# Performance work log

Measured on AMD Instinct MI355X. Metric: run time of the kernel, lower is better.

## Reference

```python
import jax, jax.numpy as jnp
import numpy as np

N_USERS = 100000
N_LOCAS = 50000
N = N_USERS + N_LOCAS
D = 128   # embedding_dynamic_size
K = 128   # kg entity dim
S = 128   # static dim
NK = 50000  # kg rows
E = 2048  # number of events
LN_EPS = 1e-5
NORM_EPS = 1e-12


def setup_inputs() -> dict:
    key = jax.random.key(0)
    ks = jax.random.split(key, 24)
    f = jnp.float32
    rin = D + K + 1
    s_rnn = 1.0 / np.sqrt(D)
    s_pred = 1.0 / np.sqrt(2 * S + 2 * D + K)
    inp = {
        'embedding': jax.random.normal(ks[0], (N, D), f),
        'static': jax.random.normal(ks[1], (N, S), f),
        'kg': jax.random.normal(ks[2], (NK, K), f),
        'W_ih_u': jax.random.normal(ks[3], (D, rin), f) * s_rnn,
        'b_ih_u': jax.random.normal(ks[4], (D,), f) * s_rnn,
        'W_hh_u': jax.random.normal(ks[5], (D, D), f) * s_rnn,
        'b_hh_u': jax.random.normal(ks[6], (D,), f) * s_rnn,
        'W_ih_l': jax.random.normal(ks[7], (D, rin), f) * s_rnn,
        'b_ih_l': jax.random.normal(ks[8], (D,), f) * s_rnn,
        'W_hh_l': jax.random.normal(ks[9], (D, D), f) * s_rnn,
        'b_hh_l': jax.random.normal(ks[10], (D,), f) * s_rnn,
        'w_proj': jax.random.normal(ks[11], (D,), f),   # NormalLinear(1, D) weight, std=1/sqrt(1)=1
        'b_proj': jax.random.normal(ks[12], (D,), f),
        'ln_g': jnp.ones((D + K,), f),
        'ln_b': jnp.zeros((D + K,), f),
        'W_pred': jax.random.normal(ks[13], (S + D, 2 * S + 2 * D + K), f) * s_pred,
        'b_pred': jnp.zeros((S + D,), f),
        'delta_u': jax.random.uniform(ks[14], (E,), f),
        'delta_l': jax.random.uniform(ks[15], (E,), f),
        'idx_user': jax.random.randint(ks[16], (E,), 0, N_USERS, jnp.int32),
        'idx_loca': jax.random.randint(ks[17], (E,), 0, N_LOCAS, jnp.int32),
        'idx_prev': jax.random.randint(ks[18], (E,), 0, N_LOCAS, jnp.int32),
        'idx_know': jax.random.randint(ks[19], (E,), 0, NK, jnp.int32),
        'num_users': N_USERS,
    }
    return inp


def reference(embedding, static, kg, W_ih_u, b_ih_u, W_hh_u, b_hh_u,
              W_ih_l, b_ih_l, W_hh_l, b_hh_l, w_proj, b_proj, ln_g, ln_b,
              W_pred, b_pred, delta_u, delta_l,
              idx_user, idx_loca, idx_prev, idx_know, num_users):
    sg = jax.lax.stop_gradient

    def l2n(x):  # F.normalize along the feature dim (row vector)
        return x / jnp.maximum(jnp.linalg.norm(x), NORM_EPS)

    # event index preprocessing (matches idx_loca + num_users etc.)
    xs = (idx_user, idx_loca + num_users, idx_prev + num_users, idx_know,
          delta_u, delta_l)

    def step(carry, ev):
        emb, loss = carry
        iu, il, ip, ik, du, dl = ev
        u = emb[iu]        # [D]
        l = emb[il]        # [D]
        p = emb[ip]        # [D]
        kgr = kg[ik]       # [K]
        # projection: u * (1 + Linear(1->D)(delta_u))
        proj = u * (1.0 + w_proj * du + b_proj)
        # layer_norm over concat([emb_prev, kg_row]) of size D+K
        x = jnp.concatenate([p, kgr])
        mu = x.mean()
        var = jnp.mean((x - mu) ** 2)
        ln = (x - mu) / jnp.sqrt(var + LN_EPS) * ln_g + ln_b
        meta = jnp.concatenate([proj, ln, static[ip], static[iu]])  # [2S+2D+K]
        pred = W_pred @ meta + b_pred                               # [S+D]
        tgt = jnp.concatenate([l, static[il]])
        loss_pred = jnp.mean((pred - sg(tgt)) ** 2)
        # RNNCell updates (tanh), then L2-normalize
        x_u = jnp.concatenate([l, kgr, du[None]])
        new_u = l2n(jnp.tanh(W_ih_u @ x_u + b_ih_u + W_hh_u @ u + b_hh_u))
        x_l = jnp.concatenate([u, kgr, dl[None]])
        new_l = l2n(jnp.tanh(W_ih_l @ x_l + b_ih_l + W_hh_l @ l + b_hh_l))
        loss = loss + loss_pred \
                    + jnp.mean((new_u - sg(u)) ** 2) \
                    + jnp.mean((new_l - sg(l)) ** 2)
        emb = emb.at[iu].set(new_u).at[il].set(new_l)
        return (emb, loss), None

    (emb, loss), _ = jax.lax.scan(
        step, (embedding, jnp.asarray(0.0, embedding.dtype)), xs)
    return emb, loss
```

## Files before the change

### kernel.cpp

```cpp
#include <hip/hip_runtime.h>

#define DEVINL static __device__ __forceinline__

typedef float f32x4 __attribute__((ext_vector_type(4)));

constexpr int NUSER = 100000;
constexpr int D     = 128;
constexpr int METAN = 640;
constexpr int NT    = 256;
constexpr int CH    = 4;
constexpr int KP4   = 160;
constexpr int KR4   = 96;
constexpr int NCPY  = 2048;
constexpr int NINIT = 512;
constexpr int CIW   = 20;

struct Params {
  const float *emb_in, *stat, *kg;
  const float *Wihu, *bihu, *Whhu, *bhhu;
  const float *Wihl, *bihl, *Whhl, *bhhl;
  const float *wproj, *bproj, *lng, *lnb, *Wpred, *bpred;
  const float *deltau, *deltal;
  const int *idxu, *idxl, *idxp, *idxk;
  float *emb;
  float *loss_slot;
  float *WpredT;
  float *WrnnT;
  float *brnn;
  float *wcol;
  float *loss_ev;
  int *cinfo;
  int *cnt_u, *cnt_w, *cnt_t;
  int *flag_u, *flag_l;
  int E, N, NLOC, NWORK;
};

DEVINL float loadx(const float* p) {
  return __hip_atomic_load(p, __ATOMIC_RELAXED, __HIP_MEMORY_SCOPE_AGENT);
}
DEVINL void storex(float* p, float v) {
  __hip_atomic_store(p, v, __ATOMIC_RELAXED, __HIP_MEMORY_SCOPE_AGENT);
}
DEVINL int loadcnt(const int* p) {
  return __hip_atomic_load(p, __ATOMIC_RELAXED, __HIP_MEMORY_SCOPE_AGENT);
}
DEVINL void sigadd(int* pp) {
  __hip_atomic_fetch_add(pp, 1, __ATOMIC_RELAXED, __HIP_MEMORY_SCOPE_AGENT);
}
DEVINL float dot4(float4 a, float4 b) { return a.x*b.x + a.y*b.y + a.z*b.z + a.w*b.w; }

DEVINL float4 block_sum4(float4 v, float4* s4) {
  #pragma unroll
  for (int o = 32; o; o >>= 1) {
    v.x += __shfl_xor(v.x, o, 64); v.y += __shfl_xor(v.y, o, 64);
    v.z += __shfl_xor(v.z, o, 64); v.w += __shfl_xor(v.w, o, 64);
  }
  if ((threadIdx.x & 63) == 0) s4[threadIdx.x >> 6] = v;
  __syncthreads();
  float4 r;
  r.x = s4[0].x + s4[1].x + s4[2].x + s4[3].x;
  r.y = s4[0].y + s4[1].y + s4[2].y + s4[3].y;
  r.z = s4[0].z + s4[1].z + s4[2].z + s4[3].z;
  r.w = s4[0].w + s4[1].w + s4[2].w + s4[3].w;
  __syncthreads();
  return r;
}

DEVINL void half_sum4(float4 v, float4* s4, float4* lo, float4* hi) {
  #pragma unroll
  for (int o = 32; o; o >>= 1) {
    v.x += __shfl_xor(v.x, o, 64); v.y += __shfl_xor(v.y, o, 64);
    v.z += __shfl_xor(v.z, o, 64); v.w += __shfl_xor(v.w, o, 64);
  }
  if ((threadIdx.x & 63) == 0) s4[threadIdx.x >> 6] = v;
  __syncthreads();
  lo->x = s4[0].x + s4[1].x; lo->y = s4[0].y + s4[1].y;
  lo->z = s4[0].z + s4[1].z; lo->w = s4[0].w + s4[1].w;
  hi->x = s4[2].x + s4[3].x; hi->y = s4[2].y + s4[3].y;
  hi->z = s4[2].z + s4[3].z; hi->w = s4[2].w + s4[3].w;
  __syncthreads();
}

__global__ __launch_bounds__(NT) void k_prep(Params p) {
  const int tid = threadIdx.x, w = tid >> 6, lane = tid & 63;
  const int bid = blockIdx.x;

  if (bid >= p.NWORK) {
    int gid = (bid - p.NWORK) * NT + tid;
    int stride = NINIT * NT;
    for (int e = gid; e < p.E; e += stride) {
      p.flag_u[p.idxu[e]] = 1;
      p.flag_l[p.idxl[e]] = 1;
    }
    for (int idx = gid; idx < 256 * KP4; idx += stride) {
      int j = idx / KP4, k4 = idx - j * KP4;
      float4 v = *(const float4*)(p.Wpred + (size_t)j * METAN + k4 * 4);
      ((float4*)p.WpredT)[k4 * 256 + j] = v;
    }
    for (int idx = gid; idx < 256 * KR4; idx += stride) {
      int j = idx / KR4, k4 = idx - j * KR4;
      int i = j & 127;
      const float* Wih = (j < 128) ? p.Wihu : p.Wihl;
      const float* Whh = (j < 128) ? p.Whhu : p.Whhl;
      float4 v; float* vp = (float*)&v;
      #pragma unroll
      for (int e = 0; e < 4; ++e) {
        int k = k4 * 4 + e;
        vp[e] = (k < 256) ? Wih[(size_t)i * 257 + k] : Whh[(size_t)i * 128 + (k - 256)];
      }
      ((float4*)p.WrnnT)[k4 * 256 + j] = v;
    }
    for (int j = gid; j < 256; j += stride) {
      int i = j & 127;
      p.brnn[j] = (j < 128) ? p.bihu[i] + p.bhhu[i] : p.bihl[i] + p.bhhl[i];
      p.wcol[j] = (j < 128) ? p.Wihu[(size_t)i * 257 + 256] : p.Wihl[(size_t)i * 257 + 256];
    }
    return;
  }

  __shared__ unsigned long long s_redu[4][CH];
  const int c = bid, base = c * CH;
  const int nev = min(CH, p.E - base);
  if (nev <= 0) return;

  int iu_[CH], il_[CH], ip_[CH];
  #pragma unroll
  for (int e = 0; e < CH; ++e) {
    int t = base + e; bool v = e < nev;
    iu_[e] = v ? p.idxu[t] : -1;
    il_[e] = v ? p.idxl[t] : -1;
    ip_[e] = v ? p.idxp[t] : -1;
  }
  unsigned long long pk[CH] = {0ull,0ull,0ull,0ull};
  for (int s = tid; s < base; s += NT) {
    int ius = p.idxu[s], ils = p.idxl[s], ips = p.idxp[s];
    #pragma unroll
    for (int e = 0; e < CH; ++e) {
      unsigned long long a  = (ius == iu_[e]);
      unsigned long long wl = (ils == il_[e]);
      unsigned long long b  = (unsigned long long)((ils == il_[e]) + (ips == il_[e]));
      unsigned long long cc = (ils == ip_[e]);
      pk[e] += a | (wl << 16) | (b << 32) | (cc << 48);
    }
  }
  #pragma unroll
  for (int o = 32; o; o >>= 1) {
    #pragma unroll
    for (int e = 0; e < CH; ++e) pk[e] += __shfl_xor(pk[e], o, 64);
  }
  if (lane == 0) {
    #pragma unroll
    for (int e = 0; e < CH; ++e) s_redu[w][e] = pk[e];
  }
  __syncthreads();
  #pragma unroll
  for (int e = 0; e < CH; ++e)
    pk[e] = s_redu[0][e] + s_redu[1][e] + s_redu[2][e] + s_redu[3][e];

  if (tid == 0) {
    int* ci = p.cinfo + (size_t)c * CIW;
    bool internal = false;
    #pragma unroll
    for (int t2 = 1; t2 < CH; ++t2) if (t2 < nev) {
      #pragma unroll
      for (int s2 = 0; s2 < t2; ++s2)
        internal |= (iu_[s2] == iu_[t2]) | (il_[s2] == il_[t2]) |
                    (il_[s2] == ip_[t2]) | (ip_[s2] == il_[t2]);
    }
    bool clean = !internal;
    #pragma unroll
    for (int e = 0; e < CH; ++e) {
      int a  = (int)(pk[e] & 0xffff),        wl = (int)((pk[e] >> 16) & 0xffff);
      int b  = (int)((pk[e] >> 32) & 0xffff), cc = (int)((pk[e] >> 48) & 0xffff);
      #pragma unroll
      for (int s2 = 0; s2 < CH; ++s2) if (s2 < e) {
        a  += (iu_[s2] == iu_[e]);
        wl += (il_[s2] == il_[e]);
        b  += (il_[s2] == il_[e]) + (ip_[s2] == il_[e]);
        cc += (il_[s2] == ip_[e]);
      }
      ci[e] = a; ci[4 + e] = wl; ci[8 + e] = b; ci[12 + e] = cc;
      if (e < nev) clean = clean && (a == 0) && (b == 0) && (cc == 0);
    }
    ci[16] = internal ? 1 : 0;
    ci[17] = clean ? 1 : 0;
  }
}

__global__ __launch_bounds__(NT, 2) void k_main(Params p) {
  const int tid = threadIdx.x, w = tid >> 6, lane = tid & 63;
  const int bid = blockIdx.x;

  if (bid >= p.NWORK) {
    size_t gid = (size_t)(bid - p.NWORK) * NT + tid;
    size_t gs  = (size_t)NCPY * NT;
    size_t n4  = (size_t)p.N * 32;
    const f32x4* src = (const f32x4*)p.emb_in;
    f32x4* dst = (f32x4*)p.emb;
    size_t g = gid;
    for (; g + 3 * gs < n4; g += 4 * gs) {
      size_t g0 = g, g1 = g + gs, g2 = g + 2 * gs, g3 = g + 3 * gs;
      int r0 = (int)(g0 >> 5), r1 = (int)(g1 >> 5), r2 = (int)(g2 >> 5), r3 = (int)(g3 >> 5);
      int f0 = (r0 < NUSER) ? p.flag_u[r0] : p.flag_l[r0 - NUSER];
      int f1 = (r1 < NUSER) ? p.flag_u[r1] : p.flag_l[r1 - NUSER];
      int f2 = (r2 < NUSER) ? p.flag_u[r2] : p.flag_l[r2 - NUSER];
      int f3 = (r3 < NUSER) ? p.flag_u[r3] : p.flag_l[r3 - NUSER];
      f32x4 v0 = src[g0], v1 = src[g1], v2 = src[g2], v3 = src[g3];
      if (!f0) dst[g0] = v0;
      if (!f1) dst[g1] = v1;
      if (!f2) dst[g2] = v2;
      if (!f3) dst[g3] = v3;
    }
    for (; g < n4; g += gs) {
      int r = (int)(g >> 5);
      int f = (r < NUSER) ? p.flag_u[r] : p.flag_l[r - NUSER];
      f32x4 v = src[g];
      if (!f) dst[g] = v;
    }
    return;
  }

  __shared__ __align__(16) float s_meta[CH][METAN];
  __shared__ __align__(16) float s_u[CH][D], s_l[CH][D], s_p[CH][D], s_kg[CH][D], s_sil[CH][D];
  __shared__ float4 s_r4[4];
  __shared__ int s_ev[8][CH];
  __shared__ float s_dd[2][CH];

  const int c = bid, base = c * CH;
  const int nev = min(CH, p.E - base);
  if (nev <= 0) return;
  const int* ci = p.cinfo + (size_t)c * CIW;
  const int internal = ci[16];
  const int clean    = ci[17];

  if (tid == 0) {
    #pragma unroll
    for (int e = 0; e < CH; ++e) {
      int t = base + e; bool v = e < nev;
      s_ev[0][e] = v ? p.idxu[t] : 0;
      s_ev[1][e] = v ? p.idxl[t] : 0;
      s_ev[2][e] = v ? p.idxp[t] : 0;
      s_ev[3][e] = ci[e];
      s_ev[4][e] = ci[4 + e];
      s_ev[5][e] = ci[8 + e];
      s_ev[6][e] = ci[12 + e];
      s_ev[7][e] = v ? p.idxk[t] : 0;
      s_dd[0][e] = v ? p.deltau[t] : 0.f;
      s_dd[1][e] = v ? p.deltal[t] : 0.f;
    }
  }
  __syncthreads();

  if (w < nev) {
    int e = w;
    int iu = s_ev[0][e], ilr = s_ev[1][e] + NUSER, ipr = s_ev[2][e] + NUSER;
    int A = s_ev[3][e], WL = s_ev[4][e], Ck = s_ev[6][e], ik = s_ev[7][e];
    int h2 = lane >> 5, li = (lane & 31) * 4;
    if (h2 == 0) {
      *(float4*)&s_kg[e][li]         = *(const float4*)(p.kg   + (size_t)ik  * D + li);
      *(float4*)&s_meta[e][512 + li] = *(const float4*)(p.stat + (size_t)iu  * D + li);
    } else {
      *(float4*)&s_meta[e][384 + li] = *(const float4*)(p.stat + (size_t)ipr * D + li);
      *(float4*)&s_sil[e][li]        = *(const float4*)(p.stat + (size_t)ilr * D + li);
    }
    int i0 = lane * 2;
    if (!A)  *(float2*)&s_u[e][i0] = *(const float2*)(p.emb_in + (size_t)iu  * D + i0);
    if (!WL) *(float2*)&s_l[e][i0] = *(const float2*)(p.emb_in + (size_t)ilr * D + i0);
    if (!Ck) *(float2*)&s_p[e][i0] = *(const float2*)(p.emb_in + (size_t)ipr * D + i0);
  }

  auto SPIN = [&](int b0, int b1) {
    if (w == 0) {
      int e = b0 + lane;
      bool act = lane < (b1 - b0);
      int iu = 0, il = 0, ip = 0, A = 0, Bc = 0, Cc = 0;
      if (act) {
        iu = s_ev[0][e]; il = s_ev[1][e]; ip = s_ev[2][e];
        A = s_ev[3][e]; Bc = s_ev[5][e]; Cc = s_ev[6][e];
      }
      int guard = 0;
      while (true) {
        int x = loadcnt(&p.cnt_u[iu]);
        int y = loadcnt(&p.cnt_t[il]);
        int z = loadcnt(&p.cnt_w[ip]);
        bool ok = (!act) | ((x >= A) & (y >= Bc) & (z >= Cc));
        if (__all(ok)) break;
        if (++guard > (1 << 22)) break;
        __builtin_amdgcn_s_sleep(1);
      }
    }
    __syncthreads();
  };

  auto POSTLOAD = [&](int b0, int b1) {
    int e = w;
    if (e >= b0 && e < b1) {
      int iu = s_ev[0][e], ilr = s_ev[1][e] + NUSER, ipr = s_ev[2][e] + NUSER;
      int A = s_ev[3][e], WL = s_ev[4][e], Ck = s_ev[6][e];
      int i0 = lane * 2;
      if (A) {
        s_u[e][i0]   = loadx(p.emb + (size_t)iu * D + i0);
        s_u[e][i0+1] = loadx(p.emb + (size_t)iu * D + i0 + 1);
      }
      if (WL) {
        s_l[e][i0]   = loadx(p.emb + (size_t)ilr * D + i0);
        s_l[e][i0+1] = loadx(p.emb + (size_t)ilr * D + i0 + 1);
      }
      if (Ck) {
        s_p[e][i0]   = loadx(p.emb + (size_t)ipr * D + i0);
        s_p[e][i0+1] = loadx(p.emb + (size_t)ipr * D + i0 + 1);
      }
    }
  };

  float nvkeep[CH] = {0.f, 0.f, 0.f, 0.f};
  const bool uc = (tid < 128);

  auto RNNPROC = [&](int b0, int b1) {
    __syncthreads();
    const float4* xo0 = (const float4*)(uc ? s_l[0] : s_u[0]);
    const float4* xo1 = (const float4*)(uc ? s_l[1] : s_u[1]);
    const float4* xo2 = (const float4*)(uc ? s_l[2] : s_u[2]);
    const float4* xo3 = (const float4*)(uc ? s_l[3] : s_u[3]);
    const float4* xk0 = (const float4*)s_kg[0];
    const float4* xk1 = (const float4*)s_kg[1];
    const float4* xk2 = (const float4*)s_kg[2];
    const float4* xk3 = (const float4*)s_kg[3];
    const float4* xs0 = (const float4*)(uc ? s_u[0] : s_l[0]);
    const float4* xs1 = (const float4*)(uc ? s_u[1] : s_l[1]);
    const float4* xs2 = (const float4*)(uc ? s_u[2] : s_l[2]);
    const float4* xs3 = (const float4*)(uc ? s_u[3] : s_l[3]);
    float ra0 = 0.f, ra1 = 0.f, ra2 = 0.f, ra3 = 0.f;
    const float4* wr = (const float4*)p.WrnnT + tid;
    #pragma unroll 8
    for (int k4 = 0; k4 < 32; ++k4) {
      float4 wv = wr[k4 * 256];
      ra0 += dot4(wv, xo0[k4]); ra1 += dot4(wv, xo1[k4]);
      ra2 += dot4(wv, xo2[k4]); ra3 += dot4(wv, xo3[k4]);
    }
    #pragma unroll 8
    for (int k4 = 32; k4 < 64; ++k4) {
      float4 wv = wr[k4 * 256];
      ra0 += dot4(wv, xk0[k4-32]); ra1 += dot4(wv, xk1[k4-32]);
      ra2 += dot4(wv, xk2[k4-32]); ra3 += dot4(wv, xk3[k4-32]);
    }
    #pragma unroll 8
    for (int k4 = 64; k4 < 96; ++k4) {
      float4 wv = wr[k4 * 256];
      ra0 += dot4(wv, xs0[k4-64]); ra1 += dot4(wv, xs1[k4-64]);
      ra2 += dot4(wv, xs2[k4-64]); ra3 += dot4(wv, xs3[k4-64]);
    }
    float brn = p.brnn[tid], wcv = p.wcol[tid];
    float d0 = uc ? s_dd[0][0] : s_dd[1][0];
    float d1 = uc ? s_dd[0][1] : s_dd[1][1];
    float d2 = uc ? s_dd[0][2] : s_dd[1][2];
    float d3 = uc ? s_dd[0][3] : s_dd[1][3];
    float h0 = tanhf(ra0 + brn + wcv * d0), h1 = tanhf(ra1 + brn + wcv * d1);
    float h2v = tanhf(ra2 + brn + wcv * d2), h3 = tanhf(ra3 + brn + wcv * d3);

    float4 SU, SL;
    half_sum4(make_float4(h0*h0, h1*h1, h2v*h2v, h3*h3), s_r4, &SU, &SL);
    float s0 = uc ? SU.x : SL.x, s1 = uc ? SU.y : SL.y;
    float s2 = uc ? SU.z : SL.z, s3 = uc ? SU.w : SL.w;
    float n0 = h0 / fmaxf(sqrtf(s0), 1e-12f), n1 = h1 / fmaxf(sqrtf(s1), 1e-12f);
    float n2 = h2v / fmaxf(sqrtf(s2), 1e-12f), n3 = h3 / fmaxf(sqrtf(s3), 1e-12f);

    if (b0 <= 0 && 0 < b1) nvkeep[0] = n0;
    if (b0 <= 1 && 1 < b1) nvkeep[1] = n1;
    if (b0 <= 2 && 2 < b1) nvkeep[2] = n2;
    if (b0 <= 3 && 3 < b1) nvkeep[3] = n3;

    float nv[CH] = {n0, n1, n2, n3};
    #pragma unroll
    for (int e = 0; e < CH; ++e) if (e >= b0 && e < b1) {
      if (tid < 128) storex(p.emb + (size_t)s_ev[0][e] * D + tid, nv[e]);
      else           storex(p.emb + ((size_t)s_ev[1][e] + NUSER) * D + (tid - 128), nv[e]);
    }
    __syncthreads();

    if (tid >= b0 && tid < b1) {
      __builtin_amdgcn_fence(__ATOMIC_RELEASE, "agent");
      sigadd(&p.cnt_u[s_ev[0][tid]]);
      sigadd(&p.cnt_t[s_ev[1][tid]]);
      sigadd(&p.cnt_w[s_ev[1][tid]]);
      sigadd(&p.cnt_t[s_ev[2][tid]]);
    }
  };

  if (clean) {
    RNNPROC(0, nev);
  } else if (!internal) {
    SPIN(0, nev);
    POSTLOAD(0, nev);
    RNNPROC(0, nev);
  } else {
    #pragma unroll
    for (int e = 0; e < CH; ++e) {
      if (e < nev) {
        SPIN(e, e + 1);
        POSTLOAD(e, e + 1);
        RNNPROC(e, e + 1);
      }
    }
  }

  if (w < nev) {
    int e = w;
    float du = s_dd[0][e];
    float4 xv = (lane < 32) ? *(const float4*)&s_p[e][lane * 4]
                            : *(const float4*)&s_kg[e][(lane - 32) * 4];
    float sm = xv.x + xv.y + xv.z + xv.w;
    #pragma unroll
    for (int o = 32; o; o >>= 1) sm += __shfl_xor(sm, o, 64);
    float mu = sm * (1.f / 256.f);
    float4 d = make_float4(xv.x - mu, xv.y - mu, xv.z - mu, xv.w - mu);
    float vs = d.x*d.x + d.y*d.y + d.z*d.z + d.w*d.w;
    #pragma unroll
    for (int o = 32; o; o >>= 1) vs += __shfl_xor(vs, o, 64);
    float rstd = rsqrtf(vs * (1.f / 256.f) + 1e-5f);
    int idx2 = lane * 4;
    float4 g  = *(const float4*)&p.lng[idx2];
    float4 bb = *(const float4*)&p.lnb[idx2];
    *(float4*)&s_meta[e][128 + idx2] = make_float4(
      d.x*rstd*g.x + bb.x, d.y*rstd*g.y + bb.y,
      d.z*rstd*g.z + bb.z, d.w*rstd*g.w + bb.w);
    int i0 = lane * 2;
    #pragma unroll
    for (int j = 0; j < 2; ++j) {
      int i = i0 + j;
      s_meta[e][i] = s_u[e][i] * (1.f + p.wproj[i] * du + p.bproj[i]);
    }
  }
  __syncthreads();

  const float4* m40 = (const float4*)&s_meta[0][0];
  const float4* m41 = (const float4*)&s_meta[1][0];
  const float4* m42 = (const float4*)&s_meta[2][0];
  const float4* m43 = (const float4*)&s_meta[3][0];
  float pa0 = 0.f, pa1 = 0.f, pa2 = 0.f, pa3 = 0.f;
  const float4* wp = (const float4*)p.WpredT + tid;
  #pragma unroll 8
  for (int k4 = 0; k4 < KP4; ++k4) {
    float4 wv = wp[k4 * 256];
    pa0 += dot4(wv, m40[k4]); pa1 += dot4(wv, m41[k4]);
    pa2 += dot4(wv, m42[k4]); pa3 += dot4(wv, m43[k4]);
  }
  float bp = p.bpred[tid];
  float4 ep2;
  {
    float tg0 = uc ? s_l[0][tid] : s_sil[0][tid - 128];
    float tg1 = uc ? s_l[1][tid] : s_sil[1][tid - 128];
    float tg2 = uc ? s_l[2][tid] : s_sil[2][tid - 128];
    float tg3 = uc ? s_l[3][tid] : s_sil[3][tid - 128];
    float e0 = pa0 + bp - tg0, e1 = pa1 + bp - tg1;
    float e2 = pa2 + bp - tg2, e3 = pa3 + bp - tg3;
    ep2 = make_float4(e0*e0, e1*e1, e2*e2, e3*e3);
  }
  float4 LP = block_sum4(ep2, s_r4);

  float o0 = uc ? s_u[0][tid] : s_l[0][tid - 128];
  float o1 = uc ? s_u[1][tid] : s_l[1][tid - 128];
  float o2 = uc ? s_u[2][tid] : s_l[2][tid - 128];
  float o3 = uc ? s_u[3][tid] : s_l[3][tid - 128];
  float q0 = nvkeep[0] - o0, q1 = nvkeep[1] - o1;
  float q2 = nvkeep[2] - o2, q3 = nvkeep[3] - o3;
  float4 LE = block_sum4(make_float4(q0*q0, q1*q1, q2*q2, q3*q3), s_r4);

  if (tid < nev) {
    float lp = (tid == 0) ? LP.x : (tid == 1) ? LP.y : (tid == 2) ? LP.z : LP.w;
    float le = (tid == 0) ? LE.x : (tid == 1) ? LE.y : (tid == 2) ? LE.z : LE.w;
    p.loss_ev[base + tid] = lp * (1.f / 256.f) + le * (1.f / 128.f);
  }
}

__global__ void k_fin(Params p) {
  __shared__ float4 s_r4[4];
  float v = 0.f;
  for (int i = threadIdx.x; i < p.E; i += NT) v += p.loss_ev[i];
  float4 r = block_sum4(make_float4(v, 0.f, 0.f, 0.f), s_r4);
  if (threadIdx.x == 0) p.loss_slot[0] = r.x;
}

extern "C" void kernel_launch(void* const* d_in, const int* in_sizes, int n_in,
                              void* d_out, int out_size, void* d_ws, size_t ws_size,
                              hipStream_t stream) {
  Params p;
  p.emb_in = (const float*)d_in[0];
  p.stat   = (const float*)d_in[1];
  p.kg     = (const float*)d_in[2];
  p.Wihu = (const float*)d_in[3];   p.bihu = (const float*)d_in[4];
  p.Whhu = (const float*)d_in[5];   p.bhhu = (const float*)d_in[6];
  p.Wihl = (const float*)d_in[7];   p.bihl = (const float*)d_in[8];
  p.Whhl = (const float*)d_in[9];   p.bhhl = (const float*)d_in[10];
  p.wproj = (const float*)d_in[11]; p.bproj = (const float*)d_in[12];
  p.lng  = (const float*)d_in[13];  p.lnb  = (const float*)d_in[14];
  p.Wpred = (const float*)d_in[15]; p.bpred = (const float*)d_in[16];
  p.deltau = (const float*)d_in[17];
  p.deltal = (const float*)d_in[18];
  p.idxu = (const int*)d_in[19];
  p.idxl = (const int*)d_in[20];
  p.idxp = (const int*)d_in[21];
  p.idxk = (const int*)d_in[22];

  p.E    = in_sizes[17];
  p.N    = in_sizes[0] / D;
  p.NLOC = p.N - NUSER;
  p.NWORK = (p.E + CH - 1) / CH;

  p.emb       = (float*)d_out;
  p.loss_slot = (float*)d_out + (size_t)p.N * D;

  char* ws = (char*)d_ws;
  size_t off = 0;
  auto take = [&](size_t bytes) {
    void* r = ws + off;
    off += (bytes + 255) & ~(size_t)255;
    return r;
  };
  p.WpredT  = (float*)take((size_t)KP4 * 256 * 16);
  p.WrnnT   = (float*)take((size_t)KR4 * 256 * 16);
  p.brnn    = (float*)take(256 * 4);
  p.wcol    = (float*)take(256 * 4);
  p.loss_ev = (float*)take((size_t)p.E * 4);
  p.cinfo   = (int*)take((size_t)p.NWORK * CIW * 4);
  size_t z0 = off;
  p.cnt_u   = (int*)take((size_t)NUSER * 4);
  p.cnt_w   = (int*)take((size_t)p.NLOC * 4);
  p.cnt_t   = (int*)take((size_t)p.NLOC * 4);
  p.flag_u  = (int*)take((size_t)NUSER * 4);
  p.flag_l  = (int*)take((size_t)p.NLOC * 4);
  size_t zbytes = off - z0;

  hipMemsetAsync(ws + z0, 0, zbytes, stream);
  hipLaunchKernelGGL(k_prep, dim3(p.NWORK + NINIT), dim3(NT), 0, stream, p);
  hipLaunchKernelGGL(k_main, dim3(p.NWORK + NCPY),  dim3(NT), 0, stream, p);
  hipLaunchKernelGGL(k_fin,  dim3(1),               dim3(NT), 0, stream, p);
}
```

Before: 151.5 us.

## Split prediction-loss work into separate blocks off the recurrent critical path

Worker blocks now do only the RNN update and dependency signalling. They stash their inputs and new states to a workspace buffer and set a per-chunk done flag. A second set of blocks waits on that flag, reloads the stash, and computes the layer norm, the prediction matvec and the losses, so that work no longer delays the serial chain of dependent events. The copy grid is halved to make room for the extra blocks. This adds stash traffic and spin-waiting blocks that occupy CUs, and the design relies on worker blocks being scheduled before the loss blocks.

```diff
diff --git a/kernel.cpp b/kernel.cpp
--- a/kernel.cpp
+++ b/kernel.cpp
@@ -11,8 +11,9 @@
 constexpr int CH    = 4;
 constexpr int KP4   = 160;
 constexpr int KR4   = 96;
-constexpr int NCPY  = 2048;
+constexpr int NCPY  = 1024;
 constexpr int NINIT = 512;
+constexpr int STW   = 640;
 constexpr int CIW   = 20;
 
 struct Params {
@@ -29,9 +30,11 @@
   float *brnn;
   float *wcol;
   float *loss_ev;
+  float *stash;
   int *cinfo;
   int *cnt_u, *cnt_w, *cnt_t;
   int *flag_u, *flag_l;
+  int *done;
   int E, N, NLOC, NWORK;
 };
 
@@ -43,6 +46,9 @@
 }
 DEVINL int loadcnt(const int* p) {
   return __hip_atomic_load(p, __ATOMIC_RELAXED, __HIP_MEMORY_SCOPE_AGENT);
+}
+DEVINL void storei(int* p, int v) {
+  __hip_atomic_store(p, v, __ATOMIC_RELAXED, __HIP_MEMORY_SCOPE_AGENT);
 }
 DEVINL void sigadd(int* pp) {
   __hip_atomic_fetch_add(pp, 1, __ATOMIC_RELAXED, __HIP_MEMORY_SCOPE_AGENT);
@@ -188,10 +194,16 @@
 }
 
 __global__ __launch_bounds__(NT, 2) void k_main(Params p) {
+  __shared__ __align__(16) float s_meta[CH][METAN];
+  __shared__ __align__(16) float s_u[CH][D], s_l[CH][D], s_p[CH][D], s_kg[CH][D], s_sil[CH][D];
+  __shared__ float4 s_r4[4];
+  __shared__ int s_ev[8][CH];
+  __shared__ float s_dd[2][CH];
+
   const int tid = threadIdx.x, w = tid >> 6, lane = tid & 63;
   const int bid = blockIdx.x;
 
-  if (bid >= p.NWORK) {
+  if (bid >= p.NWORK && bid < p.NWORK + NCPY) {
     size_t gid = (size_t)(bid - p.NWORK) * NT + tid;
     size_t gs  = (size_t)NCPY * NT;
     size_t n4  = (size_t)p.N * 32;
@@ -220,256 +232,300 @@
     return;
   }
 
-  __shared__ __align__(16) float s_meta[CH][METAN];
-  __shared__ __align__(16) float s_u[CH][D], s_l[CH][D], s_p[CH][D], s_kg[CH][D], s_sil[CH][D];
-  __shared__ float4 s_r4[4];
-  __shared__ int s_ev[8][CH];
-  __shared__ float s_dd[2][CH];
-
-  const int c = bid, base = c * CH;
+  const bool is_worker = (bid < p.NWORK);
+  const int c = is_worker ? bid : bid - p.NWORK - NCPY;
+  const int base = c * CH;
   const int nev = min(CH, p.E - base);
   if (nev <= 0) return;
-  const int* ci = p.cinfo + (size_t)c * CIW;
-  const int internal = ci[16];
-  const int clean    = ci[17];
-
-  if (tid == 0) {
-    #pragma unroll
-    for (int e = 0; e < CH; ++e) {
-      int t = base + e; bool v = e < nev;
-      s_ev[0][e] = v ? p.idxu[t] : 0;
-      s_ev[1][e] = v ? p.idxl[t] : 0;
-      s_ev[2][e] = v ? p.idxp[t] : 0;
-      s_ev[3][e] = ci[e];
-      s_ev[4][e] = ci[4 + e];
-      s_ev[5][e] = ci[8 + e];
-      s_ev[6][e] = ci[12 + e];
-      s_ev[7][e] = v ? p.idxk[t] : 0;
-      s_dd[0][e] = v ? p.deltau[t] : 0.f;
-      s_dd[1][e] = v ? p.deltal[t] : 0.f;
-    }
-  }
-  __syncthreads();
-
-  if (w < nev) {
-    int e = w;
-    int iu = s_ev[0][e], ilr = s_ev[1][e] + NUSER, ipr = s_ev[2][e] + NUSER;
-    int A = s_ev[3][e], WL = s_ev[4][e], Ck = s_ev[6][e], ik = s_ev[7][e];
-    int h2 = lane >> 5, li = (lane & 31) * 4;
-    if (h2 == 0) {
-      *(float4*)&s_kg[e][li]         = *(const float4*)(p.kg   + (size_t)ik  * D + li);
-      *(float4*)&s_meta[e][512 + li] = *(const float4*)(p.stat + (size_t)iu  * D + li);
+
+  if (is_worker) {
+    const int* ci = p.cinfo + (size_t)c * CIW;
+    const int internal = ci[16];
+    const int clean    = ci[17];
+
+    if (tid == 0) {
+      #pragma unroll
+      for (int e = 0; e < CH; ++e) {
+        int t = base + e; bool v = e < nev;
+        s_ev[0][e] = v ? p.idxu[t] : 0;
+        s_ev[1][e] = v ? p.idxl[t] : 0;
+        s_ev[2][e] = v ? p.idxp[t] : 0;
+        s_ev[3][e] = ci[e];
+        s_ev[4][e] = ci[4 + e];
+        s_ev[5][e] = ci[8 + e];
+        s_ev[6][e] = ci[12 + e];
+        s_ev[7][e] = v ? p.idxk[t] : 0;
+        s_dd[0][e] = v ? p.deltau[t] : 0.f;
+        s_dd[1][e] = v ? p.deltal[t] : 0.f;
+      }
+    }
+    __syncthreads();
+
+    if (w < nev) {
+      int e = w;
+      int iu = s_ev[0][e], ilr = s_ev[1][e] + NUSER, ipr = s_ev[2][e] + NUSER;
+      int A = s_ev[3][e], WL = s_ev[4][e], Ck = s_ev[6][e], ik = s_ev[7][e];
+      if (lane < 32) {
+        int li = lane * 4;
+        *(float4*)&s_kg[e][li] = *(const float4*)(p.kg + (size_t)ik * D + li);
+      }
+      int i0 = lane * 2;
+      if (!A)  *(float2*)&s_u[e][i0] = *(const float2*)(p.emb_in + (size_t)iu  * D + i0);
+      if (!WL) *(float2*)&s_l[e][i0] = *(const float2*)(p.emb_in + (size_t)ilr * D + i0);
+      if (!Ck) *(float2*)&s_p[e][i0] = *(const float2*)(p.emb_in + (size_t)ipr * D + i0);
+    }
+
+    auto SPIN = [&](int b0, int b1) {
+      if (w == 0) {
+        int e = b0 + lane;
+        bool act = lane < (b1 - b0);
+        int iu = 0, il = 0, ip = 0, A = 0, Bc = 0, Cc = 0;
+        if (act) {
+          iu = s_ev[0][e]; il = s_ev[1][e]; ip = s_ev[2][e];
+          A = s_ev[3][e]; Bc = s_ev[5][e]; Cc = s_ev[6][e];
+        }
+        int guard = 0;
+        while (true) {
+          int x = loadcnt(&p.cnt_u[iu]);
+          int y = loadcnt(&p.cnt_t[il]);
+          int z = loadcnt(&p.cnt_w[ip]);
+          bool ok = (!act) | ((x >= A) & (y >= Bc) & (z >= Cc));
+          if (__all(ok)) break;
+          if (++guard > (1 << 22)) break;
+          __builtin_amdgcn_s_sleep(1);
+        }
+      }
+      __syncthreads();
+    };
+
+    auto POSTLOAD = [&](int b0, int b1) {
+      int e = w;
+      if (e >= b0 && e < b1) {
+        int iu = s_ev[0][e], ilr = s_ev[1][e] + NUSER, ipr = s_ev[2][e] + NUSER;
+        int A = s_ev[3][e], WL = s_ev[4][e], Ck = s_ev[6][e];
+        int i0 = lane * 2;
+        if (A) {
+          s_u[e][i0]   = loadx(p.emb + (size_t)iu * D + i0);
+          s_u[e][i0+1] = loadx(p.emb + (size_t)iu * D + i0 + 1);
+        }
+        if (WL) {
+          s_l[e][i0]   = loadx(p.emb + (size_t)ilr * D + i0);
+          s_l[e][i0+1] = loadx(p.emb + (size_t)ilr * D + i0 + 1);
+        }
+        if (Ck) {
+          s_p[e][i0]   = loadx(p.emb + (size_t)ipr * D + i0);
+          s_p[e][i0+1] = loadx(p.emb + (size_t)ipr * D + i0 + 1);
+        }
+      }
+    };
+
+    const bool uc = (tid < 128);
+    auto RNNPROC = [&](int b0, int b1) {
+      __syncthreads();
+      const float4* xo0 = (const float4*)(uc ? s_l[0] : s_u[0]);
+      const float4* xo1 = (const float4*)(uc ? s_l[1] : s_u[1]);
+      const float4* xo2 = (const float4*)(uc ? s_l[2] : s_u[2]);
+      const float4* xo3 = (const float4*)(uc ? s_l[3] : s_u[3]);
+      const float4* xk0 = (const float4*)s_kg[0];
+      const float4* xk1 = (const float4*)s_kg[1];
+      const float4* xk2 = (const float4*)s_kg[2];
+      const float4* xk3 = (const float4*)s_kg[3];
+      const float4* xs0 = (const float4*)(uc ? s_u[0] : s_l[0]);
+      const float4* xs1 = (const float4*)(uc ? s_u[1] : s_l[1]);
+      const float4* xs2 = (const float4*)(uc ? s_u[2] : s_l[2]);
+      const float4* xs3 = (const float4*)(uc ? s_u[3] : s_l[3]);
+      float ra0 = 0.f, ra1 = 0.f, ra2 = 0.f, ra3 = 0.f;
+      const float4* wr = (const float4*)p.WrnnT + tid;
+      #pragma unroll 8
+      for (int k4 = 0; k4 < 32; ++k4) {
+        float4 wv = wr[k4 * 256];
+        ra0 += dot4(wv, xo0[k4]); ra1 += dot4(wv, xo1[k4]);
+        ra2 += dot4(wv, xo2[k4]); ra3 += dot4(wv, xo3[k4]);
+      }
+      #pragma unroll 8
+      for (int k4 = 32; k4 < 64; ++k4) {
+        float4 wv = wr[k4 * 256];
+        ra0 += dot4(wv, xk0[k4-32]); ra1 += dot4(wv, xk1[k4-32]);
+        ra2 += dot4(wv, xk2[k4-32]); ra3 += dot4(wv, xk3[k4-32]);
+      }
+      #pragma unroll 8
+      for (int k4 = 64; k4 < 96; ++k4) {
+        float4 wv = wr[k4 * 256];
+        ra0 += dot4(wv, xs0[k4-64]); ra1 += dot4(wv, xs1[k4-64]);
+        ra2 += dot4(wv, xs2[k4-64]); ra3 += dot4(wv, xs3[k4-64]);
+      }
+      float brn = p.brnn[tid], wcv = p.wcol[tid];
+      float d0 = uc ? s_dd[0][0] : s_dd[1][0];
+      float d1 = uc ? s_dd[0][1] : s_dd[1][1];
+      float d2 = uc ? s_dd[0][2] : s_dd[1][2];
+      float d3 = uc ? s_dd[0][3] : s_dd[1][3];
+      float h0 = tanhf(ra0 + brn + wcv * d0), h1 = tanhf(ra1 + brn + wcv * d1);
+      float h2v = tanhf(ra2 + brn + wcv * d2), h3 = tanhf(ra3 + brn + wcv * d3);
+
+      float4 SU, SL;
+      half_sum4(make_float4(h0*h0, h1*h1, h2v*h2v, h3*h3), s_r4, &SU, &SL);
+      float s0 = uc ? SU.x : SL.x, s1 = uc ? SU.y : SL.y;
+      float s2 = uc ? SU.z : SL.z, s3 = uc ? SU.w : SL.w;
+      float n0 = h0 / fmaxf(sqrtf(s0), 1e-12f), n1 = h1 / fmaxf(sqrtf(s1), 1e-12f);
+      float n2 = h2v / fmaxf(sqrtf(s2), 1e-12f), n3 = h3 / fmaxf(sqrtf(s3), 1e-12f);
+
+      float nv[CH] = {n0, n1, n2, n3};
+      #pragma unroll
+      for (int e = 0; e < CH; ++e) if (e >= b0 && e < b1) {
+        if (tid < 128) storex(p.emb + (size_t)s_ev[0][e] * D + tid, nv[e]);
+        else           storex(p.emb + ((size_t)s_ev[1][e] + NUSER) * D + (tid - 128), nv[e]);
+      }
+      __syncthreads();
+
+      if (tid >= b0 && tid < b1) {
+        __builtin_amdgcn_fence(__ATOMIC_RELEASE, "agent");
+        sigadd(&p.cnt_u[s_ev[0][tid]]);
+        sigadd(&p.cnt_t[s_ev[1][tid]]);
+        sigadd(&p.cnt_w[s_ev[1][tid]]);
+        sigadd(&p.cnt_t[s_ev[2][tid]]);
+      }
+
+      #pragma unroll
+      for (int e = 0; e < CH; ++e) if (e >= b0 && e < b1) {
+        float* st = p.stash + (size_t)(base + e) * STW;
+        if (tid < 128) {
+          storex(st + tid,       s_u[e][tid]);
+          storex(st + 256 + tid, s_p[e][tid]);
+          storex(st + 384 + tid, nv[e]);
+        } else {
+          int i = tid - 128;
+          storex(st + 128 + i, s_l[e][i]);
+          storex(st + 512 + i, nv[e]);
+        }
+      }
+    };
+
+    if (clean) {
+      RNNPROC(0, nev);
+    } else if (!internal) {
+      SPIN(0, nev);
+      POSTLOAD(0, nev);
+      RNNPROC(0, nev);
     } else {
-      *(float4*)&s_meta[e][384 + li] = *(const float4*)(p.stat + (size_t)ipr * D + li);
-      *(float4*)&s_sil[e][li]        = *(const float4*)(p.stat + (size_t)ilr * D + li);
-    }
-    int i0 = lane * 2;
-    if (!A)  *(float2*)&s_u[e][i0] = *(const float2*)(p.emb_in + (size_t)iu  * D + i0);
-    if (!WL) *(float2*)&s_l[e][i0] = *(const float2*)(p.emb_in + (size_t)ilr * D + i0);
-    if (!Ck) *(float2*)&s_p[e][i0] = *(const float2*)(p.emb_in + (size_t)ipr * D + i0);
-  }
-
-  auto SPIN = [&](int b0, int b1) {
-    if (w == 0) {
-      int e = b0 + lane;
-      bool act = lane < (b1 - b0);
-      int iu = 0, il = 0, ip = 0, A = 0, Bc = 0, Cc = 0;
-      if (act) {
-        iu = s_ev[0][e]; il = s_ev[1][e]; ip = s_ev[2][e];
-        A = s_ev[3][e]; Bc = s_ev[5][e]; Cc = s_ev[6][e];
-      }
-      int guard = 0;
-      while (true) {
-        int x = loadcnt(&p.cnt_u[iu]);
-        int y = loadcnt(&p.cnt_t[il]);
-        int z = loadcnt(&p.cnt_w[ip]);
-        bool ok = (!act) | ((x >= A) & (y >= Bc) & (z >= Cc));
-        if (__all(ok)) break;
-        if (++guard > (1 << 22)) break;
-        __builtin_amdgcn_s_sleep(1);
-      }
-    }
-    __syncthreads();
-  };
-
-  auto POSTLOAD = [&](int b0, int b1) {
-    int e = w;
-    if (e >= b0 && e < b1) {
-      int iu = s_ev[0][e], ilr = s_ev[1][e] + NUSER, ipr = s_ev[2][e] + NUSER;
-      int A = s_ev[3][e], WL = s_ev[4][e], Ck = s_ev[6][e];
-      int i0 = lane * 2;
-      if (A) {
-        s_u[e][i0]   = loadx(p.emb + (size_t)iu * D + i0);
-        s_u[e][i0+1] = loadx(p.emb + (size_t)iu * D + i0 + 1);
-      }
-      if (WL) {
-        s_l[e][i0]   = loadx(p.emb + (size_t)ilr * D + i0);
-        s_l[e][i0+1] = loadx(p.emb + (size_t)ilr * D + i0 + 1);
-      }
-      if (Ck) {
-        s_p[e][i0]   = loadx(p.emb + (size_t)ipr * D + i0);
-        s_p[e][i0+1] = loadx(p.emb + (size_t)ipr * D + i0 + 1);
-      }
-    }
-  };
-
-  float nvkeep[CH] = {0.f, 0.f, 0.f, 0.f};
-  const bool uc = (tid < 128);
-
-  auto RNNPROC = [&](int b0, int b1) {
-    __syncthreads();
-    const float4* xo0 = (const float4*)(uc ? s_l[0] : s_u[0]);
-    const float4* xo1 = (const float4*)(uc ? s_l[1] : s_u[1]);
-    const float4* xo2 = (const float4*)(uc ? s_l[2] : s_u[2]);
-    const float4* xo3 = (const float4*)(uc ? s_l[3] : s_u[3]);
-    const float4* xk0 = (const float4*)s_kg[0];
-    const float4* xk1 = (const float4*)s_kg[1];
-    const float4* xk2 = (const float4*)s_kg[2];
-    const float4* xk3 = (const float4*)s_kg[3];
-    const float4* xs0 = (const float4*)(uc ? s_u[0] : s_l[0]);
-    const float4* xs1 = (const float4*)(uc ? s_u[1] : s_l[1]);
-    const float4* xs2 = (const float4*)(uc ? s_u[2] : s_l[2]);
-    const float4* xs3 = (const float4*)(uc ? s_u[3] : s_l[3]);
-    float ra0 = 0.f, ra1 = 0.f, ra2 = 0.f, ra3 = 0.f;
-    const float4* wr = (const float4*)p.WrnnT + tid;
-    #pragma unroll 8
-    for (int k4 = 0; k4 < 32; ++k4) {
-      float4 wv = wr[k4 * 256];
-      ra0 += dot4(wv, xo0[k4]); ra1 += dot4(wv, xo1[k4]);
-      ra2 += dot4(wv, xo2[k4]); ra3 += dot4(wv, xo3[k4]);
-    }
-    #pragma unroll 8
-    for (int k4 = 32; k4 < 64; ++k4) {
-      float4 wv = wr[k4 * 256];
-      ra0 += dot4(wv, xk0[k4-32]); ra1 += dot4(wv, xk1[k4-32]);
-      ra2 += dot4(wv, xk2[k4-32]); ra3 += dot4(wv, xk3[k4-32]);
-    }
-    #pragma unroll 8
-    for (int k4 = 64; k4 < 96; ++k4) {
-      float4 wv = wr[k4 * 256];
-      ra0 += dot4(wv, xs0[k4-64]); ra1 += dot4(wv, xs1[k4-64]);
-      ra2 += dot4(wv, xs2[k4-64]); ra3 += dot4(wv, xs3[k4-64]);
-    }
-    float brn = p.brnn[tid], wcv = p.wcol[tid];
-    float d0 = uc ? s_dd[0][0] : s_dd[1][0];
-    float d1 = uc ? s_dd[0][1] : s_dd[1][1];
-    float d2 = uc ? s_dd[0][2] : s_dd[1][2];
-    float d3 = uc ? s_dd[0][3] : s_dd[1][3];
-    float h0 = tanhf(ra0 + brn + wcv * d0), h1 = tanhf(ra1 + brn + wcv * d1);
-    float h2v = tanhf(ra2 + brn + wcv * d2), h3 = tanhf(ra3 + brn + wcv * d3);
-
-    float4 SU, SL;
-    half_sum4(make_float4(h0*h0, h1*h1, h2v*h2v, h3*h3), s_r4, &SU, &SL);
-    float s0 = uc ? SU.x : SL.x, s1 = uc ? SU.y : SL.y;
-    float s2 = uc ? SU.z : SL.z, s3 = uc ? SU.w : SL.w;
-    float n0 = h0 / fmaxf(sqrtf(s0), 1e-12f), n1 = h1 / fmaxf(sqrtf(s1), 1e-12f);
-    float n2 = h2v / fmaxf(sqrtf(s2), 1e-12f), n3 = h3 / fmaxf(sqrtf(s3), 1e-12f);
-
-    if (b0 <= 0 && 0 < b1) nvkeep[0] = n0;
-    if (b0 <= 1 && 1 < b1) nvkeep[1] = n1;
-    if (b0 <= 2 && 2 < b1) nvkeep[2] = n2;
-    if (b0 <= 3 && 3 < b1) nvkeep[3] = n3;
-
-    float nv[CH] = {n0, n1, n2, n3};
-    #pragma unroll
-    for (int e = 0; e < CH; ++e) if (e >= b0 && e < b1) {
-      if (tid < 128) storex(p.emb + (size_t)s_ev[0][e] * D + tid, nv[e]);
-      else           storex(p.emb + ((size_t)s_ev[1][e] + NUSER) * D + (tid - 128), nv[e]);
-    }
-    __syncthreads();
-
-    if (tid >= b0 && tid < b1) {
-      __builtin_amdgcn_fence(__ATOMIC_RELEASE, "agent");
-      sigadd(&p.cnt_u[s_ev[0][tid]]);
-      sigadd(&p.cnt_t[s_ev[1][tid]]);
-      sigadd(&p.cnt_w[s_ev[1][tid]]);
-      sigadd(&p.cnt_t[s_ev[2][tid]]);
-    }
-  };
-
-  if (clean) {
-    RNNPROC(0, nev);
-  } else if (!internal) {
-    SPIN(0, nev);
-    POSTLOAD(0, nev);
-    RNNPROC(0, nev);
-  } else {
-    #pragma unroll
-    for (int e = 0; e < CH; ++e) {
-      if (e < nev) {
+      #pragma unroll
+      for (int e = 0; e < CH; ++e) if (e < nev) {
         SPIN(e, e + 1);
         POSTLOAD(e, e + 1);
         RNNPROC(e, e + 1);
       }
     }
-  }
-
-  if (w < nev) {
-    int e = w;
-    float du = s_dd[0][e];
-    float4 xv = (lane < 32) ? *(const float4*)&s_p[e][lane * 4]
-                            : *(const float4*)&s_kg[e][(lane - 32) * 4];
-    float sm = xv.x + xv.y + xv.z + xv.w;
-    #pragma unroll
-    for (int o = 32; o; o >>= 1) sm += __shfl_xor(sm, o, 64);
-    float mu = sm * (1.f / 256.f);
-    float4 d = make_float4(xv.x - mu, xv.y - mu, xv.z - mu, xv.w - mu);
-    float vs = d.x*d.x + d.y*d.y + d.z*d.z + d.w*d.w;
-    #pragma unroll
-    for (int o = 32; o; o >>= 1) vs += __shfl_xor(vs, o, 64);
-    float rstd = rsqrtf(vs * (1.f / 256.f) + 1e-5f);
-    int idx2 = lane * 4;
-    float4 g  = *(const float4*)&p.lng[idx2];
-    float4 bb = *(const float4*)&p.lnb[idx2];
-    *(float4*)&s_meta[e][128 + idx2] = make_float4(
-      d.x*rstd*g.x + bb.x, d.y*rstd*g.y + bb.y,
-      d.z*rstd*g.z + bb.z, d.w*rstd*g.w + bb.w);
-    int i0 = lane * 2;
-    #pragma unroll
-    for (int j = 0; j < 2; ++j) {
-      int i = i0 + j;
-      s_meta[e][i] = s_u[e][i] * (1.f + p.wproj[i] * du + p.bproj[i]);
-    }
-  }
-  __syncthreads();
-
-  const float4* m40 = (const float4*)&s_meta[0][0];
-  const float4* m41 = (const float4*)&s_meta[1][0];
-  const float4* m42 = (const float4*)&s_meta[2][0];
-  const float4* m43 = (const float4*)&s_meta[3][0];
-  float pa0 = 0.f, pa1 = 0.f, pa2 = 0.f, pa3 = 0.f;
-  const float4* wp = (const float4*)p.WpredT + tid;
-  #pragma unroll 8
-  for (int k4 = 0; k4 < KP4; ++k4) {
-    float4 wv = wp[k4 * 256];
-    pa0 += dot4(wv, m40[k4]); pa1 += dot4(wv, m41[k4]);
-    pa2 += dot4(wv, m42[k4]); pa3 += dot4(wv, m43[k4]);
-  }
-  float bp = p.bpred[tid];
-  float4 ep2;
+    __syncthreads();
+    if (tid == 0) storei(&p.done[c], 1);
+    return;
+  }
+
   {
-    float tg0 = uc ? s_l[0][tid] : s_sil[0][tid - 128];
-    float tg1 = uc ? s_l[1][tid] : s_sil[1][tid - 128];
-    float tg2 = uc ? s_l[2][tid] : s_sil[2][tid - 128];
-    float tg3 = uc ? s_l[3][tid] : s_sil[3][tid - 128];
-    float e0 = pa0 + bp - tg0, e1 = pa1 + bp - tg1;
-    float e2 = pa2 + bp - tg2, e3 = pa3 + bp - tg3;
-    ep2 = make_float4(e0*e0, e1*e1, e2*e2, e3*e3);
-  }
-  float4 LP = block_sum4(ep2, s_r4);
-
-  float o0 = uc ? s_u[0][tid] : s_l[0][tid - 128];
-  float o1 = uc ? s_u[1][tid] : s_l[1][tid - 128];
-  float o2 = uc ? s_u[2][tid] : s_l[2][tid - 128];
-  float o3 = uc ? s_u[3][tid] : s_l[3][tid - 128];
-  float q0 = nvkeep[0] - o0, q1 = nvkeep[1] - o1;
-  float q2 = nvkeep[2] - o2, q3 = nvkeep[3] - o3;
-  float4 LE = block_sum4(make_float4(q0*q0, q1*q1, q2*q2, q3*q3), s_r4);
-
-  if (tid < nev) {
-    float lp = (tid == 0) ? LP.x : (tid == 1) ? LP.y : (tid == 2) ? LP.z : LP.w;
-    float le = (tid == 0) ? LE.x : (tid == 1) ? LE.y : (tid == 2) ? LE.z : LE.w;
-    p.loss_ev[base + tid] = lp * (1.f / 256.f) + le * (1.f / 128.f);
+    if (w == 0) {
+      int guard = 0;
+      while (!loadcnt(&p.done[c])) {
+        if (++guard > (1 << 22)) break;
+        __builtin_amdgcn_s_sleep(1);
+      }
+    }
+    __syncthreads();
+
+    if (w < nev) {
+      int e = w;
+      int t = base + e;
+      int iu = p.idxu[t], ilr = p.idxl[t] + NUSER, ipr = p.idxp[t] + NUSER, ik = p.idxk[t];
+      const float* st = p.stash + (size_t)t * STW;
+      int i0 = lane * 2;
+      s_u[e][i0]   = loadx(st + i0);
+      s_u[e][i0+1] = loadx(st + i0 + 1);
+      s_l[e][i0]   = loadx(st + 128 + i0);
+      s_l[e][i0+1] = loadx(st + 128 + i0 + 1);
+      s_p[e][i0]   = loadx(st + 256 + i0);
+      s_p[e][i0+1] = loadx(st + 256 + i0 + 1);
+      int h2 = lane >> 5, li = (lane & 31) * 4;
+      if (h2 == 0) {
+        *(float4*)&s_kg[e][li]         = *(const float4*)(p.kg   + (size_t)ik  * D + li);
+        *(float4*)&s_meta[e][512 + li] = *(const float4*)(p.stat + (size_t)iu  * D + li);
+      } else {
+        *(float4*)&s_meta[e][384 + li] = *(const float4*)(p.stat + (size_t)ipr * D + li);
+        *(float4*)&s_sil[e][li]        = *(const float4*)(p.stat + (size_t)ilr * D + li);
+      }
+    }
+    __syncthreads();
+
+    if (w < nev) {
+      int e = w;
+      float du = p.deltau[base + e];
+      float4 xv = (lane < 32) ? *(const float4*)&s_p[e][lane * 4]
+                              : *(const float4*)&s_kg[e][(lane - 32) * 4];
+      float sm = xv.x + xv.y + xv.z + xv.w;
+      #pragma unroll
+      for (int o = 32; o; o >>= 1) sm += __shfl_xor(sm, o, 64);
+      float mu = sm * (1.f / 256.f);
+      float4 d = make_float4(xv.x - mu, xv.y - mu, xv.z - mu, xv.w - mu);
+      float vs = d.x*d.x + d.y*d.y + d.z*d.z + d.w*d.w;
+      #pragma unroll
+      for (int o = 32; o; o >>= 1) vs += __shfl_xor(vs, o, 64);
+      float rstd = rsqrtf(vs * (1.f / 256.f) + 1e-5f);
+      int idx2 = lane * 4;
+      float4 g  = *(const float4*)&p.lng[idx2];
+      float4 bb = *(const float4*)&p.lnb[idx2];
+      *(float4*)&s_meta[e][128 + idx2] = make_float4(
+        d.x*rstd*g.x + bb.x, d.y*rstd*g.y + bb.y,
+        d.z*rstd*g.z + bb.z, d.w*rstd*g.w + bb.w);
+      int i0 = lane * 2;
+      #pragma unroll
+      for (int j = 0; j < 2; ++j) {
+        int i = i0 + j;
+        s_meta[e][i] = s_u[e][i] * (1.f + p.wproj[i] * du + p.bproj[i]);
+      }
+    }
+    __syncthreads();
+
+    const bool uc = (tid < 128);
+    const float4* m40 = (const float4*)&s_meta[0][0];
+    const float4* m41 = (const float4*)&s_meta[1][0];
+    const float4* m42 = (const float4*)&s_meta[2][0];
+    const float4* m43 = (const float4*)&s_meta[3][0];
+    float pa0 = 0.f, pa1 = 0.f, pa2 = 0.f, pa3 = 0.f;
+    const float4* wp = (const float4*)p.WpredT + tid;
+    #pragma unroll 8
+    for (int k4 = 0; k4 < KP4; ++k4) {
+      float4 wv = wp[k4 * 256];
+      pa0 += dot4(wv, m40[k4]); pa1 += dot4(wv, m41[k4]);
+      pa2 += dot4(wv, m42[k4]); pa3 += dot4(wv, m43[k4]);
+    }
+    float bp = p.bpred[tid];
+    float4 ep2;
+    {
+      float tg0 = uc ? s_l[0][tid] : s_sil[0][tid - 128];
+      float tg1 = uc ? s_l[1][tid] : s_sil[1][tid - 128];
+      float tg2 = uc ? s_l[2][tid] : s_sil[2][tid - 128];
+      float tg3 = uc ? s_l[3][tid] : s_sil[3][tid - 128];
+      float e0 = pa0 + bp - tg0, e1 = pa1 + bp - tg1;
+      float e2 = pa2 + bp - tg2, e3 = pa3 + bp - tg3;
+      ep2 = make_float4(e0*e0, e1*e1, e2*e2, e3*e3);
+    }
+    float4 LP = block_sum4(ep2, s_r4);
+
+    const float* st0 = p.stash + (size_t)(base + 0) * STW;
+    const float* st1 = p.stash + (size_t)(base + 1) * STW;
+    const float* st2 = p.stash + (size_t)(base + 2) * STW;
+    const float* st3 = p.stash + (size_t)(base + 3) * STW;
+    int noff = uc ? (384 + tid) : (512 + tid - 128);
+    float n0 = loadx(st0 + noff), n1 = (nev > 1) ? loadx(st1 + noff) : 0.f;
+    float n2 = (nev > 2) ? loadx(st2 + noff) : 0.f, n3 = (nev > 3) ? loadx(st3 + noff) : 0.f;
+    float o0 = uc ? s_u[0][tid] : s_l[0][tid - 128];
+    float o1 = uc ? s_u[1][tid] : s_l[1][tid - 128];
+    float o2 = uc ? s_u[2][tid] : s_l[2][tid - 128];
+    float o3 = uc ? s_u[3][tid] : s_l[3][tid - 128];
+    float q0 = n0 - o0, q1 = n1 - o1, q2 = n2 - o2, q3 = n3 - o3;
+    float4 LE = block_sum4(make_float4(q0*q0, q1*q1, q2*q2, q3*q3), s_r4);
+
+    if (tid < nev) {
+      float lp = (tid == 0) ? LP.x : (tid == 1) ? LP.y : (tid == 2) ? LP.z : LP.w;
+      float le = (tid == 0) ? LE.x : (tid == 1) ? LE.y : (tid == 2) ? LE.z : LE.w;
+      p.loss_ev[base + tid] = lp * (1.f / 256.f) + le * (1.f / 128.f);
+    }
   }
 }
 
@@ -522,6 +578,7 @@
   p.brnn    = (float*)take(256 * 4);
   p.wcol    = (float*)take(256 * 4);
   p.loss_ev = (float*)take((size_t)p.E * 4);
+  p.stash   = (float*)take((size_t)p.E * STW * 4);
   p.cinfo   = (int*)take((size_t)p.NWORK * CIW * 4);
   size_t z0 = off;
   p.cnt_u   = (int*)take((size_t)NUSER * 4);
@@ -529,10 +586,11 @@
   p.cnt_t   = (int*)take((size_t)p.NLOC * 4);
   p.flag_u  = (int*)take((size_t)NUSER * 4);
   p.flag_l  = (int*)take((size_t)p.NLOC * 4);
+  p.done    = (int*)take((size_t)p.NWORK * 4);
   size_t zbytes = off - z0;
 
   hipMemsetAsync(ws + z0, 0, zbytes, stream);
-  hipLaunchKernelGGL(k_prep, dim3(p.NWORK + NINIT), dim3(NT), 0, stream, p);
-  hipLaunchKernelGGL(k_main, dim3(p.NWORK + NCPY),  dim3(NT), 0, stream, p);
-  hipLaunchKernelGGL(k_fin,  dim3(1),               dim3(NT), 0, stream, p);
-}
+  hipLaunchKernelGGL(k_prep, dim3(p.NWORK + NINIT),          dim3(NT), 0, stream, p);
+  hipLaunchKernelGGL(k_main, dim3(p.NWORK * 2 + NCPY),       dim3(NT), 0, stream, p);
+  hipLaunchKernelGGL(k_fin,  dim3(1),                        dim3(NT), 0, stream, p);
+}
```

Result: slower. 156.5 us (+3.3%).
